# Kernel optimization log

Hardware: AMD Instinct MI355X
Metric: run time of the kernel (lower is better)

## Reference

```python
import jax, jax.numpy as jnp
import numpy as np

S, B, E, H = 1024, 4, 1024, 16
D = E // H  # head_dim = 64


def setup_inputs() -> dict:
    key = jax.random.key(0)
    ks = jax.random.split(key, 22)
    inp = {}
    names_io = ["query_r", "query_i", "key_r", "key_i", "value_r", "value_i"]
    for i, n in enumerate(names_io):
        inp[n] = jax.random.normal(ks[i], (S, B, E), dtype=jnp.float32)
    scale = 0.02
    j = 6
    for p in ["q", "k", "v", "o"]:
        inp[f"w{p}_r"] = jax.random.normal(ks[j], (E, E), dtype=jnp.float32) * scale; j += 1
        inp[f"w{p}_i"] = jax.random.normal(ks[j], (E, E), dtype=jnp.float32) * scale; j += 1
        inp[f"b{p}_r"] = jax.random.normal(ks[j], (E,), dtype=jnp.float32) * scale; j += 1
        inp[f"b{p}_i"] = jax.random.normal(ks[j], (E,), dtype=jnp.float32) * scale; j += 1
    return inp


def _clinear(x, wr, wi, br, bi):
    # complex linear: x @ W^T + b, torch Linear convention (weight [out,in])
    w = wr + 1j * wi
    b = br + 1j * bi
    return x @ w.T + b


def reference(query_r, query_i, key_r, key_i, value_r, value_i,
              wq_r, wq_i, bq_r, bq_i, wk_r, wk_i, bk_r, bk_i,
              wv_r, wv_i, bv_r, bv_i, wo_r, wo_i, bo_r, bo_i):
    # batch_first=False: inputs are [S, B, E] -> [B, S, E]
    q = jnp.transpose(query_r + 1j * query_i, (1, 0, 2))
    k = jnp.transpose(key_r + 1j * key_i, (1, 0, 2))
    v = jnp.transpose(value_r + 1j * value_i, (1, 0, 2))

    def heads(x):  # [B,S,E] -> [B,H,S,D]
        return jnp.transpose(x.reshape(B, S, H, D), (0, 2, 1, 3))

    Q = heads(_clinear(q, wq_r, wq_i, bq_r, bq_i))
    K = heads(_clinear(k, wk_r, wk_i, bk_r, bk_i))
    V = heads(_clinear(v, wv_r, wv_i, bv_r, bv_i))

    scores = jnp.einsum("bhqd,bhkd->bhqk", Q, K) / jnp.sqrt(jnp.float32(D))
    # split softmax: softmax over real and imag parts independently
    attn = (jax.nn.softmax(scores.real, axis=-1)
            + 1j * jax.nn.softmax(scores.imag, axis=-1))
    out = jnp.einsum("bhqk,bhkd->bhqd", attn, V)  # [B,H,S,D]
    out = jnp.transpose(out, (0, 2, 1, 3)).reshape(B, S, E)
    out = _clinear(out, wo_r, wo_i, bo_r, bo_i)
    out = jnp.transpose(out, (1, 0, 2))  # back to [S,B,E]
    # return complex output as stacked (real, imag) floats: [S,B,E,2]
    return jnp.stack([out.real, out.imag], axis=-1)
```

## Files before the change

kernel.cpp:

```cpp
#include <hip/hip_runtime.h>
#include <hip/hip_bf16.h>
#include <stdint.h>

#define S_LEN 1024
#define B_SZ  4
#define E_SZ  1024
#define H_CNT 16
#define D_HD  64
#define N1    (B_SZ * H_CNT * S_LEN * D_HD)
#define WELEM (E_SZ * E_SZ)

typedef __attribute__((ext_vector_type(8))) short short8;
typedef __attribute__((ext_vector_type(4))) float f32x4;

__device__ __forceinline__ ushort f2bf(float f) {
  union { float f; uint32_t u; } v; v.f = f;
  uint32_t u = v.u;
  uint32_t r = (u + 0x7fffu + ((u >> 16) & 1u)) >> 16;
  return (ushort)r;
}
__device__ __forceinline__ short8 pack8(float4 a, float4 b) {
  short8 r;
  r[0] = (short)f2bf(a.x); r[1] = (short)f2bf(a.y);
  r[2] = (short)f2bf(a.z); r[3] = (short)f2bf(a.w);
  r[4] = (short)f2bf(b.x); r[5] = (short)f2bf(b.y);
  r[6] = (short)f2bf(b.z); r[7] = (short)f2bf(b.w);
  return r;
}
static __device__ __forceinline__ f32x4 mfma16(short8 a, short8 b, f32x4 c) {
  return __builtin_amdgcn_mfma_f32_16x16x32_bf16(a, b, c, 0, 0, 0);
}

typedef const __attribute__((address_space(1))) void gv_t;
typedef __attribute__((address_space(3))) void lv_t;
__device__ __forceinline__ void gld16(const void* g, void* l) {
  __builtin_amdgcn_global_load_lds((gv_t*)g, (lv_t*)l, 16, 0, 0);
}

__global__ __launch_bounds__(256) void cast_w8(
    const float* __restrict__ s0, const float* __restrict__ s1,
    const float* __restrict__ s2, const float* __restrict__ s3,
    const float* __restrict__ s4, const float* __restrict__ s5,
    const float* __restrict__ s6, const float* __restrict__ s7,
    ushort* __restrict__ dst)
{
  const size_t i = (size_t)blockIdx.x * blockDim.x + threadIdx.x;
  const size_t e = i * 4;
  const int which = (int)(e >> 20);
  const size_t off = e & (WELEM - 1);
  const float* s = which < 4
      ? (which < 2 ? (which == 0 ? s0 : s1) : (which == 2 ? s2 : s3))
      : (which < 6 ? (which == 4 ? s4 : s5) : (which == 6 ? s6 : s7));
  const float4 f = *(const float4*)(s + off);
  ushort4 u;
  u.x = f2bf(f.x); u.y = f2bf(f.y); u.z = f2bf(f.z); u.w = f2bf(f.w);
  *(ushort4*)(dst + e) = u;
}

__global__ __launch_bounds__(256) void castA2(
    const float* __restrict__ xr0, const float* __restrict__ xi0,
    const float* __restrict__ xr1, const float* __restrict__ xi1,
    ushort* __restrict__ yr0, ushort* __restrict__ yi0,
    ushort* __restrict__ yr1, ushort* __restrict__ yi1)
{
  int blk = blockIdx.x;
  const float *xr, *xi; ushort *yr, *yi;
  if (blk < 2048) { xr = xr0; xi = xi0; yr = yr0; yi = yi0; }
  else            { xr = xr1; xi = xi1; yr = yr1; yi = yi1; blk -= 2048; }
  const size_t e = ((size_t)blk * 256 + threadIdx.x) * 8;
  float4 a = *(const float4*)(xr + e);
  float4 b = *(const float4*)(xr + e + 4);
  *(short8*)(yr + e) = pack8(a, b);
  a = *(const float4*)(xi + e);
  b = *(const float4*)(xi + e + 4);
  *(short8*)(yi + e) = pack8(a, b);
}

__global__ __launch_bounds__(256) void castA(
    const float* __restrict__ xr, const float* __restrict__ xi,
    ushort* __restrict__ yr, ushort* __restrict__ yi)
{
  const size_t e = ((size_t)blockIdx.x * 256 + threadIdx.x) * 8;
  float4 a = *(const float4*)(xr + e);
  float4 b = *(const float4*)(xr + e + 4);
  *(short8*)(yr + e) = pack8(a, b);
  a = *(const float4*)(xi + e);
  b = *(const float4*)(xi + e + 4);
  *(short8*)(yi + e) = pack8(a, b);
}

template<int MODE>
__global__ __launch_bounds__(256) void cgemm(
    const ushort* __restrict__ ar_, const ushort* __restrict__ ai_,
    const ushort* __restrict__ wre, const ushort* __restrict__ wim,
    const float* __restrict__ bre, const float* __restrict__ bim,
    ushort* __restrict__ yr, ushort* __restrict__ yi,
    float* __restrict__ outf, float scale)
{
  __shared__ __align__(16) ushort sAr[128 * 64], sAi[128 * 64];
  __shared__ __align__(16) ushort sBr[64 * 64],  sBi[64 * 64];

  const int tid  = threadIdx.x;
  const int lane = tid & 63;
  const int w    = tid >> 6;
  const int wrow = w >> 1, wcol = w & 1;
  const int fr   = lane & 15, fq = lane >> 4;

  const int flat = blockIdx.x + gridDim.x * blockIdx.y;
  const int swz  = (flat & 7) * 64 + (flat >> 3);
  const int n0   = (swz & 15) * 64;
  const int m0   = (swz >> 4) * 128;

  const ushort* gbase = (w == 0) ? ar_ : (w == 1) ? ai_ : (w == 2) ? wre : wim;
  char* sbase = (w == 0) ? (char*)sAr : (w == 1) ? (char*)sAi
              : (w == 2) ? (char*)sBr : (char*)sBi;
  const int rbase = (w < 2) ? m0 : n0;
  const int lrow  = lane >> 3;
  const int sch   = (lane & 7) ^ lrow;
  const ushort* gp0 = gbase + (size_t)(rbase + lrow) * E_SZ + sch * 8;

  f32x4 accR[4][2] = {}, accI[4][2] = {};

  for (int kt = 0; kt < 16; ++kt) {
    const int k0 = kt * 64;
    __syncthreads();
    if (w < 2) {
#pragma unroll
      for (int i = 0; i < 16; ++i)
        gld16(gp0 + (size_t)i * 8 * E_SZ + k0, sbase + i * 1024);
    } else {
#pragma unroll
      for (int i = 0; i < 8; ++i)
        gld16(gp0 + (size_t)i * 8 * E_SZ + k0, sbase + i * 1024);
    }
    __syncthreads();

#pragma unroll
    for (int kk = 0; kk < 2; ++kk) {
      short8 a_r[4], a_i[4], a_n[4], b_r[2], b_i[2];
#pragma unroll
      for (int mi = 0; mi < 4; ++mi) {
        const int row = wrow * 64 + mi * 16 + fr;
        const int off = row * 128 + (((kk * 4 + fq) ^ (row & 7)) << 4);
        a_r[mi] = *(const short8*)((const char*)sAr + off);
        a_i[mi] = *(const short8*)((const char*)sAi + off);
        a_n[mi] = a_i[mi] ^ (short)0x8000;
      }
#pragma unroll
      for (int ni = 0; ni < 2; ++ni) {
        const int row = wcol * 32 + ni * 16 + fr;
        const int off = row * 128 + (((kk * 4 + fq) ^ (row & 7)) << 4);
        b_r[ni] = *(const short8*)((const char*)sBr + off);
        b_i[ni] = *(const short8*)((const char*)sBi + off);
      }
      __builtin_amdgcn_s_setprio(1);
#pragma unroll
      for (int mi = 0; mi < 4; ++mi)
#pragma unroll
        for (int ni = 0; ni < 2; ++ni) {
          accR[mi][ni] = mfma16(a_r[mi], b_r[ni], accR[mi][ni]);
          accR[mi][ni] = mfma16(a_n[mi], b_i[ni], accR[mi][ni]);
          accI[mi][ni] = mfma16(a_r[mi], b_i[ni], accI[mi][ni]);
          accI[mi][ni] = mfma16(a_i[mi], b_r[ni], accI[mi][ni]);
        }
      __builtin_amdgcn_s_setprio(0);
    }
  }

#pragma unroll
  for (int ni = 0; ni < 2; ++ni) {
    const int n = n0 + wcol * 32 + ni * 16 + fr;
    const float bR = bre[n], bI = bim[n];
    const int h = n >> 6, d = n & 63;
#pragma unroll
    for (int mi = 0; mi < 4; ++mi) {
      const int mb = m0 + wrow * 64 + mi * 16 + fq * 4;
#pragma unroll
      for (int q = 0; q < 4; ++q) {
        const int m = mb + q;
        const float vr = (accR[mi][ni][q] + bR) * scale;
        const float vi = (accI[mi][ni][q] + bI) * scale;
        if (MODE == 0) {
          const int s = m >> 2, b = m & 3;
          const size_t o = (((size_t)(b * H_CNT + h) * S_LEN) + s) * D_HD + d;
          yr[o] = f2bf(vr); yi[o] = f2bf(vi);
        } else if (MODE == 1) {
          const int s = m >> 2, b = m & 3;
          const size_t o = (((size_t)(b * H_CNT + h) * D_HD) + d) * S_LEN + s;
          yr[o] = f2bf(vr); yi[o] = f2bf(vi);
        } else {
          const int b = m >> 10, s = m & 1023;
          const size_t o = (((size_t)(s * B_SZ + b) * E_SZ) + n) * 2;
          outf[o] = vr; outf[o + 1] = vi;
        }
      }
    }
  }
}

__global__ __launch_bounds__(256, 3) void cattn_mfma(
    const ushort* __restrict__ Qr, const ushort* __restrict__ Qi,
    const ushort* __restrict__ Kr, const ushort* __restrict__ Ki,
    const ushort* __restrict__ Vtr, const ushort* __restrict__ Vti,
    ushort* __restrict__ AOr, ushort* __restrict__ AOi)
{
  __shared__ __align__(16) ushort sK[2][64][64];
  __shared__ __align__(16) ushort sVt[2][64][64];
  __shared__ __align__(16) ushort sP[4][2][16][64];

  const int tid  = threadIdx.x;
  const int lane = tid & 63;
  const int w    = tid >> 6;
  const int g    = lane >> 4;
  const int fr   = lane & 15;
  const int bh   = blockIdx.y;
  const int b    = bh >> 4, h = bh & 15;
  const int q0   = blockIdx.x * 64;
  const int qw   = q0 + 16 * w;

  short8 qfr[2], qfi[2];
  const size_t qrow = ((size_t)bh * S_LEN + qw + fr) * D_HD;
#pragma unroll
  for (int kk = 0; kk < 2; ++kk) {
    qfr[kk] = *(const short8*)(Qr + qrow + kk * 32 + g * 8);
    qfi[kk] = *(const short8*)(Qi + qrow + kk * 32 + g * 8);
  }

  const int lrow8 = lane >> 3;
  const int sch   = (lane & 7) ^ lrow8;
  const ushort* gsrc; ushort* sdst;
  if      (w == 0) { gsrc = Kr  + (size_t)bh * S_LEN * D_HD; sdst = &sK[0][0][0]; }
  else if (w == 1) { gsrc = Ki  + (size_t)bh * S_LEN * D_HD; sdst = &sK[1][0][0]; }
  else if (w == 2) { gsrc = Vtr + (size_t)bh * D_HD * S_LEN; sdst = &sVt[0][0][0]; }
  else             { gsrc = Vti + (size_t)bh * D_HD * S_LEN; sdst = &sVt[1][0][0]; }
  const bool isK = (w < 2);

  f32x4 accA[4] = {}, accAi[4] = {}, accB[4] = {}, accBi[4] = {};
  float lpr = 0.f, lpi = 0.f;

  ushort* pR = &sP[w][0][0][0];
  ushort* pI = &sP[w][1][0][0];

  for (int kt = 0; kt < 16; ++kt) {
    __syncthreads();
    if (isK) {
      const ushort* gp = gsrc + (size_t)kt * 4096 + lrow8 * 64 + sch * 8;
#pragma unroll
      for (int i = 0; i < 8; ++i)
        gld16(gp + i * 512, (char*)sdst + i * 1024);
    } else {
      const ushort* gp = gsrc + (size_t)lrow8 * S_LEN + kt * 64 + sch * 8;
#pragma unroll
      for (int i = 0; i < 8; ++i)
        gld16(gp + (size_t)i * 8 * S_LEN, (char*)sdst + i * 1024);
    }
    __syncthreads();

    f32x4 Sr[4] = {}, Si[4] = {};
#pragma unroll
    for (int n = 0; n < 4; ++n) {
      const int kc = fr + 16 * n;
      const int rb = kc * 128, sw = (kc & 7) << 4;
#pragma unroll
      for (int kk = 0; kk < 2; ++kk) {
        const int off = rb + ((((kk * 4 + g) << 4)) ^ sw);
        short8 krf = *(const short8*)((const char*)&sK[0][0][0] + off);
        short8 kif = *(const short8*)((const char*)&sK[1][0][0] + off);
        short8 kin = kif ^ (short)0x8000;
        Sr[n] = mfma16(krf, qfr[kk], Sr[n]);
        Sr[n] = mfma16(kin, qfi[kk], Sr[n]);
        Si[n] = mfma16(kif, qfr[kk], Si[n]);
        Si[n] = mfma16(krf, qfi[kk], Si[n]);
      }
    }

    const int pbase = fr * 128 + ((g & 1) << 3);
#pragma unroll
    for (int n = 0; n < 4; ++n) {
      float p0 = __builtin_amdgcn_exp2f(Sr[n][0]);
      float p1 = __builtin_amdgcn_exp2f(Sr[n][1]);
      float p2 = __builtin_amdgcn_exp2f(Sr[n][2]);
      float p3 = __builtin_amdgcn_exp2f(Sr[n][3]);
      float q0_ = __builtin_amdgcn_exp2f(Si[n][0]);
      float q1_ = __builtin_amdgcn_exp2f(Si[n][1]);
      float q2_ = __builtin_amdgcn_exp2f(Si[n][2]);
      float q3_ = __builtin_amdgcn_exp2f(Si[n][3]);
      lpr += (p0 + p1) + (p2 + p3);
      lpi += (q0_ + q1_) + (q2_ + q3_);
      uint32_t a0, a1, b0, b1;
      asm("v_cvt_pk_bf16_f32 %0, %1, %2" : "=v"(a0) : "v"(p0), "v"(p1));
      asm("v_cvt_pk_bf16_f32 %0, %1, %2" : "=v"(a1) : "v"(p2), "v"(p3));
      asm("v_cvt_pk_bf16_f32 %0, %1, %2" : "=v"(b0) : "v"(q0_), "v"(q1_));
      asm("v_cvt_pk_bf16_f32 %0, %1, %2" : "=v"(b1) : "v"(q2_), "v"(q3_));
      const int chunk = (2 * n + (g >> 1)) ^ (fr & 7);
      const int off = pbase + (chunk << 4);
      uint2 pa; pa.x = a0; pa.y = a1;
      uint2 pb; pb.x = b0; pb.y = b1;
      *(uint2*)((char*)pR + off) = pa;
      *(uint2*)((char*)pI + off) = pb;
    }
    asm volatile("s_waitcnt lgkmcnt(0)" ::: "memory");

    short8 prf[2], pif[2];
#pragma unroll
    for (int kk = 0; kk < 2; ++kk) {
      const int off = fr * 128 + ((((kk * 4 + g) << 4)) ^ ((fr & 7) << 4));
      prf[kk] = *(const short8*)((const char*)pR + off);
      pif[kk] = *(const short8*)((const char*)pI + off);
    }
#pragma unroll
    for (int n = 0; n < 4; ++n) {
      const int d = fr + 16 * n;
      const int rb = d * 128, sw = (d & 7) << 4;
#pragma unroll
      for (int kk = 0; kk < 2; ++kk) {
        const int off = rb + ((((kk * 4 + g) << 4)) ^ sw);
        short8 vrf = *(const short8*)((const char*)&sVt[0][0][0] + off);
        short8 vif = *(const short8*)((const char*)&sVt[1][0][0] + off);
        accA [n] = mfma16(prf[kk], vrf, accA [n]);
        accAi[n] = mfma16(prf[kk], vif, accAi[n]);
        accB [n] = mfma16(pif[kk], vrf, accB [n]);
        accBi[n] = mfma16(pif[kk], vif, accBi[n]);
      }
    }
  }

  lpr += __shfl_xor(lpr, 16); lpr += __shfl_xor(lpr, 32);
  lpi += __shfl_xor(lpi, 16); lpi += __shfl_xor(lpi, 32);
  f32x4 ilr, ili;
#pragma unroll
  for (int t = 0; t < 4; ++t) {
    const int src = (lane & 48) + (g << 2) + t;
    ilr[t] = 1.f / __shfl(lpr, src, 64);
    ili[t] = 1.f / __shfl(lpi, src, 64);
  }

#pragma unroll
  for (int n = 0; n < 4; ++n) {
    const int e = h * 64 + fr + 16 * n;
#pragma unroll
    for (int t = 0; t < 4; ++t) {
      const int sidx = qw + g * 4 + t;
      const size_t o = ((size_t)b * S_LEN + sidx) * E_SZ + e;
      AOr[o] = f2bf(accA [n][t] * ilr[t] - accBi[n][t] * ili[t]);
      AOi[o] = f2bf(accAi[n][t] * ilr[t] + accB [n][t] * ili[t]);
    }
  }
}

extern "C" void kernel_launch(void* const* d_in, const int* in_sizes, int n_in,
                              void* d_out, int out_size, void* d_ws, size_t ws_size,
                              hipStream_t stream)
{
    const float* query_r = (const float*)d_in[0];
    const float* query_i = (const float*)d_in[1];
    const float* key_r   = (const float*)d_in[2];
    const float* key_i   = (const float*)d_in[3];
    const float* value_r = (const float*)d_in[4];
    const float* value_i = (const float*)d_in[5];
    const float* wq_r = (const float*)d_in[6];
    const float* wq_i = (const float*)d_in[7];
    const float* bq_r = (const float*)d_in[8];
    const float* bq_i = (const float*)d_in[9];
    const float* wk_r = (const float*)d_in[10];
    const float* wk_i = (const float*)d_in[11];
    const float* bk_r = (const float*)d_in[12];
    const float* bk_i = (const float*)d_in[13];
    const float* wv_r = (const float*)d_in[14];
    const float* wv_i = (const float*)d_in[15];
    const float* bv_r = (const float*)d_in[16];
    const float* bv_i = (const float*)d_in[17];
    const float* wo_r = (const float*)d_in[18];
    const float* wo_i = (const float*)d_in[19];
    const float* bo_r = (const float*)d_in[20];
    const float* bo_i = (const float*)d_in[21];

    ushort* ws   = (ushort*)d_ws;
    ushort* Qr   = ws;
    ushort* Qi   = Qr + (size_t)N1;
    ushort* Kr   = Qi + (size_t)N1;
    ushort* Ki   = Kr + (size_t)N1;
    ushort* Vtr  = Ki + (size_t)N1;
    ushort* Vti  = Vtr + (size_t)N1;
    ushort* Wb   = Vti + (size_t)N1;
    ushort* Wq_r = Wb + 0 * (size_t)WELEM;
    ushort* Wq_i = Wb + 1 * (size_t)WELEM;
    ushort* Wk_r = Wb + 2 * (size_t)WELEM;
    ushort* Wk_i = Wb + 3 * (size_t)WELEM;
    ushort* Wv_r = Wb + 4 * (size_t)WELEM;
    ushort* Wv_i = Wb + 5 * (size_t)WELEM;
    ushort* Wo_r = Wb + 6 * (size_t)WELEM;
    ushort* Wo_i = Wb + 7 * (size_t)WELEM;
    ushort* AOr  = Wb + 8 * (size_t)WELEM;
    ushort* AOi  = AOr + (size_t)N1;

    ushort* Xq_r = (ushort*)d_out;
    ushort* Xq_i = Xq_r + (size_t)N1;
    ushort* Xk_r = Xq_i + (size_t)N1;
    ushort* Xk_i = Xk_r + (size_t)N1;

    cast_w8<<<8192, 256, 0, stream>>>(wq_r, wq_i, wk_r, wk_i,
                                      wv_r, wv_i, wo_r, wo_i, Wb);
    castA2<<<4096, 256, 0, stream>>>(query_r, query_i, key_r, key_i,
                                     Xq_r, Xq_i, Xk_r, Xk_i);

    dim3 gg(16, 32);

    cgemm<0><<<gg, 256, 0, stream>>>(Xq_r, Xq_i, Wq_r, Wq_i, bq_r, bq_i,
                                     Qr, Qi, nullptr, 0.18033688011112043f);
    cgemm<0><<<gg, 256, 0, stream>>>(Xk_r, Xk_i, Wk_r, Wk_i, bk_r, bk_i,
                                     Kr, Ki, nullptr, 1.0f);
    castA<<<2048, 256, 0, stream>>>(value_r, value_i, Xq_r, Xq_i);
    cgemm<1><<<gg, 256, 0, stream>>>(Xq_r, Xq_i, Wv_r, Wv_i, bv_r, bv_i,
                                     Vtr, Vti, nullptr, 1.0f);

    cattn_mfma<<<dim3(S_LEN / 64, B_SZ * H_CNT), 256, 0, stream>>>(
        Qr, Qi, Kr, Ki, Vtr, Vti, AOr, AOi);

    cgemm<2><<<gg, 256, 0, stream>>>(AOr, AOi, Wo_r, Wo_i, bo_r, bo_i,
                                     nullptr, nullptr, (float*)d_out, 1.0f);
}
```

Baseline: 269.1 us.

## Batch Q/K/V projections into one launch and merge all cast kernels

Merges the three input casts and the weight cast into one kernel, and runs the Q, K and V complex GEMMs as a single launch, with blockIdx.z choosing the projection. This removes launch gaps and gives the device three times as many blocks per launch, so small GEMM grids no longer leave compute units idle. The attention grid is remapped so blocks of the same batch-head share an XCD for L2 reuse of K/V. Staging X_v in the AO buffer adds buffer aliasing, which is safe only because attention writes AO after the projections finish.

```diff
diff --git a/kernel.cpp b/kernel.cpp
--- a/kernel.cpp
+++ b/kernel.cpp
@@ -37,36 +37,39 @@
   __builtin_amdgcn_global_load_lds((gv_t*)g, (lv_t*)l, 16, 0, 0);
 }
 
-__global__ __launch_bounds__(256) void cast_w8(
+__global__ __launch_bounds__(256) void cast_all(
     const float* __restrict__ s0, const float* __restrict__ s1,
     const float* __restrict__ s2, const float* __restrict__ s3,
     const float* __restrict__ s4, const float* __restrict__ s5,
     const float* __restrict__ s6, const float* __restrict__ s7,
-    ushort* __restrict__ dst)
-{
-  const size_t i = (size_t)blockIdx.x * blockDim.x + threadIdx.x;
-  const size_t e = i * 4;
-  const int which = (int)(e >> 20);
-  const size_t off = e & (WELEM - 1);
-  const float* s = which < 4
-      ? (which < 2 ? (which == 0 ? s0 : s1) : (which == 2 ? s2 : s3))
-      : (which < 6 ? (which == 4 ? s4 : s5) : (which == 6 ? s6 : s7));
-  const float4 f = *(const float4*)(s + off);
-  ushort4 u;
-  u.x = f2bf(f.x); u.y = f2bf(f.y); u.z = f2bf(f.z); u.w = f2bf(f.w);
-  *(ushort4*)(dst + e) = u;
-}
-
-__global__ __launch_bounds__(256) void castA2(
-    const float* __restrict__ xr0, const float* __restrict__ xi0,
-    const float* __restrict__ xr1, const float* __restrict__ xi1,
-    ushort* __restrict__ yr0, ushort* __restrict__ yi0,
-    ushort* __restrict__ yr1, ushort* __restrict__ yi1)
+    ushort* __restrict__ wdst,
+    const float* __restrict__ qr, const float* __restrict__ qi,
+    const float* __restrict__ kr, const float* __restrict__ ki,
+    const float* __restrict__ vr, const float* __restrict__ vi,
+    ushort* __restrict__ xq_r, ushort* __restrict__ xq_i,
+    ushort* __restrict__ xk_r, ushort* __restrict__ xk_i,
+    ushort* __restrict__ xv_r, ushort* __restrict__ xv_i)
 {
   int blk = blockIdx.x;
+  if (blk < 8192) {
+    const size_t i = (size_t)blk * 256 + threadIdx.x;
+    const size_t e = i * 4;
+    const int which = (int)(e >> 20);
+    const size_t off = e & (WELEM - 1);
+    const float* s = which < 4
+        ? (which < 2 ? (which == 0 ? s0 : s1) : (which == 2 ? s2 : s3))
+        : (which < 6 ? (which == 4 ? s4 : s5) : (which == 6 ? s6 : s7));
+    const float4 f = *(const float4*)(s + off);
+    ushort4 u;
+    u.x = f2bf(f.x); u.y = f2bf(f.y); u.z = f2bf(f.z); u.w = f2bf(f.w);
+    *(ushort4*)(wdst + e) = u;
+    return;
+  }
+  blk -= 8192;
   const float *xr, *xi; ushort *yr, *yi;
-  if (blk < 2048) { xr = xr0; xi = xi0; yr = yr0; yi = yi0; }
-  else            { xr = xr1; xi = xi1; yr = yr1; yi = yi1; blk -= 2048; }
+  if      (blk < 2048) { xr = qr; xi = qi; yr = xq_r; yi = xq_i; }
+  else if (blk < 4096) { xr = kr; xi = ki; yr = xk_r; yi = xk_i; blk -= 2048; }
+  else                 { xr = vr; xi = vi; yr = xv_r; yi = xv_i; blk -= 4096; }
   const size_t e = ((size_t)blk * 256 + threadIdx.x) * 8;
   float4 a = *(const float4*)(xr + e);
   float4 b = *(const float4*)(xr + e + 4);
@@ -76,29 +79,34 @@
   *(short8*)(yi + e) = pack8(a, b);
 }
 
-__global__ __launch_bounds__(256) void castA(
-    const float* __restrict__ xr, const float* __restrict__ xi,
-    ushort* __restrict__ yr, ushort* __restrict__ yi)
-{
-  const size_t e = ((size_t)blockIdx.x * 256 + threadIdx.x) * 8;
-  float4 a = *(const float4*)(xr + e);
-  float4 b = *(const float4*)(xr + e + 4);
-  *(short8*)(yr + e) = pack8(a, b);
-  a = *(const float4*)(xi + e);
-  b = *(const float4*)(xi + e + 4);
-  *(short8*)(yi + e) = pack8(a, b);
-}
-
-template<int MODE>
-__global__ __launch_bounds__(256) void cgemm(
-    const ushort* __restrict__ ar_, const ushort* __restrict__ ai_,
-    const ushort* __restrict__ wre, const ushort* __restrict__ wim,
-    const float* __restrict__ bre, const float* __restrict__ bim,
-    ushort* __restrict__ yr, ushort* __restrict__ yi,
-    float* __restrict__ outf, float scale)
+__global__ __launch_bounds__(256) void cgemm_qkv3(
+    const ushort* __restrict__ a0r, const ushort* __restrict__ a0i,
+    const ushort* __restrict__ a1r, const ushort* __restrict__ a1i,
+    const ushort* __restrict__ a2r, const ushort* __restrict__ a2i,
+    const ushort* __restrict__ w0r, const ushort* __restrict__ w0i,
+    const ushort* __restrict__ w1r, const ushort* __restrict__ w1i,
+    const ushort* __restrict__ w2r, const ushort* __restrict__ w2i,
+    const float* __restrict__ b0r, const float* __restrict__ b0i,
+    const float* __restrict__ b1r, const float* __restrict__ b1i,
+    const float* __restrict__ b2r, const float* __restrict__ b2i,
+    ushort* __restrict__ y0r, ushort* __restrict__ y0i,
+    ushort* __restrict__ y1r, ushort* __restrict__ y1i,
+    ushort* __restrict__ y2r, ushort* __restrict__ y2i,
+    float qscale)
 {
   __shared__ __align__(16) ushort sAr[128 * 64], sAi[128 * 64];
   __shared__ __align__(16) ushort sBr[64 * 64],  sBi[64 * 64];
+
+  const int z = blockIdx.z;
+  const ushort* ar_ = (z == 0) ? a0r : (z == 1) ? a1r : a2r;
+  const ushort* ai_ = (z == 0) ? a0i : (z == 1) ? a1i : a2i;
+  const ushort* wre = (z == 0) ? w0r : (z == 1) ? w1r : w2r;
+  const ushort* wim = (z == 0) ? w0i : (z == 1) ? w1i : w2i;
+  const float*  bre = (z == 0) ? b0r : (z == 1) ? b1r : b2r;
+  const float*  bim = (z == 0) ? b0i : (z == 1) ? b1i : b2i;
+  ushort* yr = (z == 0) ? y0r : (z == 1) ? y1r : y2r;
+  ushort* yi = (z == 0) ? y0i : (z == 1) ? y1i : y2i;
+  const float scale = (z == 0) ? qscale : 1.0f;
 
   const int tid  = threadIdx.x;
   const int lane = tid & 63;
@@ -180,19 +188,106 @@
         const int m = mb + q;
         const float vr = (accR[mi][ni][q] + bR) * scale;
         const float vi = (accI[mi][ni][q] + bI) * scale;
-        if (MODE == 0) {
-          const int s = m >> 2, b = m & 3;
-          const size_t o = (((size_t)(b * H_CNT + h) * S_LEN) + s) * D_HD + d;
-          yr[o] = f2bf(vr); yi[o] = f2bf(vi);
-        } else if (MODE == 1) {
-          const int s = m >> 2, b = m & 3;
-          const size_t o = (((size_t)(b * H_CNT + h) * D_HD) + d) * S_LEN + s;
-          yr[o] = f2bf(vr); yi[o] = f2bf(vi);
-        } else {
-          const int b = m >> 10, s = m & 1023;
-          const size_t o = (((size_t)(s * B_SZ + b) * E_SZ) + n) * 2;
-          outf[o] = vr; outf[o + 1] = vi;
+        const int s = m >> 2, b = m & 3;
+        size_t o;
+        if (z < 2) o = (((size_t)(b * H_CNT + h) * S_LEN) + s) * D_HD + d;
+        else       o = (((size_t)(b * H_CNT + h) * D_HD) + d) * S_LEN + s;
+        yr[o] = f2bf(vr); yi[o] = f2bf(vi);
+      }
+    }
+  }
+}
+
+__global__ __launch_bounds__(256) void cgemm_o(
+    const ushort* __restrict__ ar_, const ushort* __restrict__ ai_,
+    const ushort* __restrict__ wre, const ushort* __restrict__ wim,
+    const float* __restrict__ bre, const float* __restrict__ bim,
+    float* __restrict__ outf)
+{
+  __shared__ __align__(16) ushort sAr[128 * 64], sAi[128 * 64];
+  __shared__ __align__(16) ushort sBr[64 * 64],  sBi[64 * 64];
+
+  const int tid  = threadIdx.x;
+  const int lane = tid & 63;
+  const int w    = tid >> 6;
+  const int wrow = w >> 1, wcol = w & 1;
+  const int fr   = lane & 15, fq = lane >> 4;
+
+  const int flat = blockIdx.x + gridDim.x * blockIdx.y;
+  const int swz  = (flat & 7) * 64 + (flat >> 3);
+  const int n0   = (swz & 15) * 64;
+  const int m0   = (swz >> 4) * 128;
+
+  const ushort* gbase = (w == 0) ? ar_ : (w == 1) ? ai_ : (w == 2) ? wre : wim;
+  char* sbase = (w == 0) ? (char*)sAr : (w == 1) ? (char*)sAi
+              : (w == 2) ? (char*)sBr : (char*)sBi;
+  const int rbase = (w < 2) ? m0 : n0;
+  const int lrow  = lane >> 3;
+  const int sch   = (lane & 7) ^ lrow;
+  const ushort* gp0 = gbase + (size_t)(rbase + lrow) * E_SZ + sch * 8;
+
+  f32x4 accR[4][2] = {}, accI[4][2] = {};
+
+  for (int kt = 0; kt < 16; ++kt) {
+    const int k0 = kt * 64;
+    __syncthreads();
+    if (w < 2) {
+#pragma unroll
+      for (int i = 0; i < 16; ++i)
+        gld16(gp0 + (size_t)i * 8 * E_SZ + k0, sbase + i * 1024);
+    } else {
+#pragma unroll
+      for (int i = 0; i < 8; ++i)
+        gld16(gp0 + (size_t)i * 8 * E_SZ + k0, sbase + i * 1024);
+    }
+    __syncthreads();
+
+#pragma unroll
+    for (int kk = 0; kk < 2; ++kk) {
+      short8 a_r[4], a_i[4], a_n[4], b_r[2], b_i[2];
+#pragma unroll
+      for (int mi = 0; mi < 4; ++mi) {
+        const int row = wrow * 64 + mi * 16 + fr;
+        const int off = row * 128 + (((kk * 4 + fq) ^ (row & 7)) << 4);
+        a_r[mi] = *(const short8*)((const char*)sAr + off);
+        a_i[mi] = *(const short8*)((const char*)sAi + off);
+        a_n[mi] = a_i[mi] ^ (short)0x8000;
+      }
+#pragma unroll
+      for (int ni = 0; ni < 2; ++ni) {
+        const int row = wcol * 32 + ni * 16 + fr;
+        const int off = row * 128 + (((kk * 4 + fq) ^ (row & 7)) << 4);
+        b_r[ni] = *(const short8*)((const char*)sBr + off);
+        b_i[ni] = *(const short8*)((const char*)sBi + off);
+      }
+      __builtin_amdgcn_s_setprio(1);
+#pragma unroll
+      for (int mi = 0; mi < 4; ++mi)
+#pragma unroll
+        for (int ni = 0; ni < 2; ++ni) {
+          accR[mi][ni] = mfma16(a_r[mi], b_r[ni], accR[mi][ni]);
+          accR[mi][ni] = mfma16(a_n[mi], b_i[ni], accR[mi][ni]);
+          accI[mi][ni] = mfma16(a_r[mi], b_i[ni], accI[mi][ni]);
+          accI[mi][ni] = mfma16(a_i[mi], b_r[ni], accI[mi][ni]);
         }
+      __builtin_amdgcn_s_setprio(0);
+    }
+  }
+
+#pragma unroll
+  for (int ni = 0; ni < 2; ++ni) {
+    const int n = n0 + wcol * 32 + ni * 16 + fr;
+    const float bR = bre[n], bI = bim[n];
+#pragma unroll
+    for (int mi = 0; mi < 4; ++mi) {
+      const int mb = m0 + wrow * 64 + mi * 16 + fq * 4;
+#pragma unroll
+      for (int q = 0; q < 4; ++q) {
+        const int m = mb + q;
+        const int b = m >> 10, s = m & 1023;
+        const size_t o = (((size_t)(s * B_SZ + b) * E_SZ) + n) * 2;
+        outf[o]     = accR[mi][ni][q] + bR;
+        outf[o + 1] = accI[mi][ni][q] + bI;
       }
     }
   }
@@ -213,9 +308,13 @@
   const int w    = tid >> 6;
   const int g    = lane >> 4;
   const int fr   = lane & 15;
-  const int bh   = blockIdx.y;
+
+  const int id   = blockIdx.x;
+  const int xcd  = id & 7;
+  const int loc  = id >> 3;
+  const int bh   = (xcd << 3) | (loc & 7);
+  const int q0   = (loc >> 3) << 6;
   const int b    = bh >> 4, h = bh & 15;
-  const int q0   = blockIdx.x * 64;
   const int qw   = q0 + 16 * w;
 
   short8 qfr[2], qfi[2];
@@ -398,25 +497,25 @@
     ushort* Xq_i = Xq_r + (size_t)N1;
     ushort* Xk_r = Xq_i + (size_t)N1;
     ushort* Xk_i = Xk_r + (size_t)N1;
-
-    cast_w8<<<8192, 256, 0, stream>>>(wq_r, wq_i, wk_r, wk_i,
-                                      wv_r, wv_i, wo_r, wo_i, Wb);
-    castA2<<<4096, 256, 0, stream>>>(query_r, query_i, key_r, key_i,
-                                     Xq_r, Xq_i, Xk_r, Xk_i);
-
-    dim3 gg(16, 32);
-
-    cgemm<0><<<gg, 256, 0, stream>>>(Xq_r, Xq_i, Wq_r, Wq_i, bq_r, bq_i,
-                                     Qr, Qi, nullptr, 0.18033688011112043f);
-    cgemm<0><<<gg, 256, 0, stream>>>(Xk_r, Xk_i, Wk_r, Wk_i, bk_r, bk_i,
-                                     Kr, Ki, nullptr, 1.0f);
-    castA<<<2048, 256, 0, stream>>>(value_r, value_i, Xq_r, Xq_i);
-    cgemm<1><<<gg, 256, 0, stream>>>(Xq_r, Xq_i, Wv_r, Wv_i, bv_r, bv_i,
-                                     Vtr, Vti, nullptr, 1.0f);
-
-    cattn_mfma<<<dim3(S_LEN / 64, B_SZ * H_CNT), 256, 0, stream>>>(
+    ushort* Xv_r = AOr;
+    ushort* Xv_i = AOi;
+
+    cast_all<<<14336, 256, 0, stream>>>(
+        wq_r, wq_i, wk_r, wk_i, wv_r, wv_i, wo_r, wo_i, Wb,
+        query_r, query_i, key_r, key_i, value_r, value_i,
+        Xq_r, Xq_i, Xk_r, Xk_i, Xv_r, Xv_i);
+
+    dim3 gg3(16, 32, 3);
+    cgemm_qkv3<<<gg3, 256, 0, stream>>>(
+        Xq_r, Xq_i, Xk_r, Xk_i, Xv_r, Xv_i,
+        Wq_r, Wq_i, Wk_r, Wk_i, Wv_r, Wv_i,
+        bq_r, bq_i, bk_r, bk_i, bv_r, bv_i,
+        Qr, Qi, Kr, Ki, Vtr, Vti,
+        0.18033688011112043f);
+
+    cattn_mfma<<<1024, 256, 0, stream>>>(
         Qr, Qi, Kr, Ki, Vtr, Vti, AOr, AOi);
 
-    cgemm<2><<<gg, 256, 0, stream>>>(AOr, AOi, Wo_r, Wo_i, bo_r, bo_i,
-                                     nullptr, nullptr, (float*)d_out, 1.0f);
-}
+    cgemm_o<<<dim3(16, 32), 256, 0, stream>>>(
+        AOr, AOi, Wo_r, Wo_i, bo_r, bo_i, (float*)d_out);
+}
```

Result: faster. 262.5 us (-2.4%).
